# Performance work log

Hardware: AMD Instinct MI355X
Metric: run time of the kernel (lower is better)

Reference implementation:

```python
import jax, jax.numpy as jnp
import numpy as np
import math

B, S, H, D = 4, 4096, 2048, 128  # batch, seq_len, hidden_dim, head_size

def setup_inputs() -> dict:
    key = jax.random.key(0)
    ks = jax.random.split(key, 7)
    scale = 1.0 / math.sqrt(H)
    return {
        "x": jax.random.normal(ks[0], (B, S, H), dtype=jnp.float32),
        "Wq": jax.random.normal(ks[1], (H, D), dtype=jnp.float32) * scale,
        "bq": jnp.zeros((D,), dtype=jnp.float32),
        "Wk": jax.random.normal(ks[2], (H, D), dtype=jnp.float32) * scale,
        "bk": jnp.zeros((D,), dtype=jnp.float32),
        "Wv": jax.random.normal(ks[3], (H, D), dtype=jnp.float32) * scale,
        "bv": jnp.zeros((D,), dtype=jnp.float32),
    }

def reference(x, Wq, bq, Wk, bk, Wv, bv):
    # projections: [B,S,D]
    q = x @ Wq + bq
    k = x @ Wk + bk
    v = x @ Wv + bv
    # raw scores [B,S,S] with causal mask, NO pre-softmax scaling (as in source)
    scores = jnp.einsum('bsd,btd->bst', q, k)
    causal = jnp.tril(jnp.ones((S, S), dtype=bool))
    scores = jnp.where(causal, scores, -jnp.inf)
    # non-standard: scale AFTER softmax by 1/sqrt(head_size)
    w = jax.nn.softmax(scores, axis=-1) * (1.0 / math.sqrt(D))
    # dropout p=0.0 -> identity
    return jnp.einsum('bst,btd->bsd', w, v)
```

## Files before the change

### kernel.cpp

```cpp
#include <hip/hip_runtime.h>
#include <math.h>
#include <stdint.h>

#define SEQ   4096
#define HID   2048
#define HD    128
#define NROWS 16384

typedef __attribute__((ext_vector_type(8))) short bf16x8;
typedef __attribute__((ext_vector_type(4))) float f32x4;

static constexpr float OSCALE = 0.088388347648318447f;

using gvptr = const __attribute__((address_space(1))) void*;
using lvptr = __attribute__((address_space(3))) void*;
__device__ __forceinline__ void gld_lds16(const void* g, void* l) {
    __builtin_amdgcn_global_load_lds((gvptr)g, (lvptr)l, 16, 0, 0);
}

__device__ __forceinline__ unsigned short f2bf_rne(float f) {
    union { float f; unsigned u; } v; v.f = f;
    unsigned u = v.u + 0x7fffu + ((v.u >> 16) & 1u);
    return (unsigned short)(u >> 16);
}
__device__ __forceinline__ unsigned short f2bf_tr(float f) {
    union { float f; unsigned u; } v; v.f = f;
    return (unsigned short)(v.u >> 16);
}
__device__ __forceinline__ float bf2f(unsigned short h) {
    union { unsigned u; float f; } v; v.u = ((unsigned)h) << 16;
    return v.f;
}

__global__ __launch_bounds__(256) void prep_w(
    const float* __restrict__ Wq, const float* __restrict__ Wk, const float* __restrict__ Wv,
    unsigned short* __restrict__ wth, unsigned short* __restrict__ wtl)
{
    __shared__ float T[64][68];
    const int tid = threadIdx.x;
    const int k0 = blockIdx.x * 64, n0 = blockIdx.y * 64, mm = blockIdx.z;
    const float* W = (mm == 0) ? Wq : (mm == 1) ? Wk : Wv;
    #pragma unroll
    for (int i = 0; i < 4; ++i) {
        const int fi = i * 256 + tid, kk = fi >> 4, nc = (fi & 15) * 4;
        const float4 w = *(const float4*)(W + (size_t)(k0 + kk) * HD + n0 + nc);
        T[kk][nc] = w.x; T[kk][nc + 1] = w.y; T[kk][nc + 2] = w.z; T[kk][nc + 3] = w.w;
    }
    __syncthreads();
    unsigned short* oh = wth + (size_t)mm * HD * HID;
    unsigned short* ol = wtl + (size_t)mm * HD * HID;
    #pragma unroll
    for (int i = 0; i < 4; ++i) {
        const int fi = i * 256 + tid, nn = fi >> 4, kc = (fi & 15) * 4;
        const float a = T[kc][nn], b = T[kc + 1][nn], c = T[kc + 2][nn], d = T[kc + 3][nn];
        ushort4 hv, lv;
        hv.x = f2bf_rne(a); hv.y = f2bf_rne(b); hv.z = f2bf_rne(c); hv.w = f2bf_rne(d);
        lv.x = f2bf_rne(a - bf2f(hv.x)); lv.y = f2bf_rne(b - bf2f(hv.y));
        lv.z = f2bf_rne(c - bf2f(hv.z)); lv.w = f2bf_rne(d - bf2f(hv.w));
        *(ushort4*)(oh + (size_t)(n0 + nn) * HID + k0 + kc) = hv;
        *(ushort4*)(ol + (size_t)(n0 + nn) * HID + k0 + kc) = lv;
    }
}

__global__ __launch_bounds__(256, 3) void qkv_split(
    const float* __restrict__ x,
    const float* __restrict__ bq, const float* __restrict__ bk, const float* __restrict__ bv,
    const unsigned short* __restrict__ wth, const unsigned short* __restrict__ wtl,
    unsigned short* __restrict__ qh, unsigned short* __restrict__ ql,
    unsigned short* __restrict__ kh, unsigned short* __restrict__ kl,
    unsigned short* __restrict__ vth)
{
    __shared__ unsigned short Ah[64][64], Al[64][64];
    __shared__ unsigned short Bh[128][64], Bl[128][64];

    const int tid = threadIdx.x, wave = tid >> 6, lane = tid & 63;
    const int l15 = lane & 15, q4 = lane >> 4;
    const int wr = wave >> 1, wc = wave & 1;
    const int type = blockIdx.x % 3;
    const int tile = blockIdx.x / 3;
    const int r0 = tile * 64;
    const bool qk = (type < 2);

    const unsigned short* wh = wth + (size_t)type * HD * HID;
    const unsigned short* wl = wtl + (size_t)type * HD * HID;

    const int srow   = lane >> 3;
    const int schunk = ((lane & 7) ^ srow) * 8;

    f32x4 acc[2][4];
    #pragma unroll
    for (int mt = 0; mt < 2; ++mt)
        #pragma unroll
        for (int nt = 0; nt < 4; ++nt)
            acc[mt][nt] = (f32x4){0.f, 0.f, 0.f, 0.f};

    const float* xbase = x + (size_t)r0 * HID;

    float4 xv[4];
    #pragma unroll
    for (int i = 0; i < 4; ++i) {
        const int fi = i * 256 + tid, row = fi >> 4, kc = (fi & 15) * 4;
        xv[i] = *(const float4*)(xbase + (size_t)row * HID + kc);
    }

    for (int k0 = 0; k0 < HID; k0 += 64) {
        __syncthreads();

        {
            #pragma unroll
            for (int c = 0; c < 4; ++c) {
                const int row = wave * 32 + c * 8;
                gld_lds16(wh + (size_t)(row + srow) * HID + k0 + schunk, &Bh[row][0]);
            }
            if (qk) {
                #pragma unroll
                for (int c = 0; c < 4; ++c) {
                    const int row = wave * 32 + c * 8;
                    gld_lds16(wl + (size_t)(row + srow) * HID + k0 + schunk, &Bl[row][0]);
                }
            }
        }
        #pragma unroll
        for (int i = 0; i < 4; ++i) {
            const int fi = i * 256 + tid, row = fi >> 4, kc = (fi & 15) * 4;
            const int pk = ((kc >> 3) ^ (row & 7)) * 8 + (kc & 7);
            ushort4 hv;
            hv.x = f2bf_tr(xv[i].x); hv.y = f2bf_tr(xv[i].y);
            hv.z = f2bf_tr(xv[i].z); hv.w = f2bf_tr(xv[i].w);
            *(ushort4*)&Ah[row][pk] = hv;
            if (qk) {
                ushort4 lv;
                lv.x = f2bf_tr(xv[i].x - bf2f(hv.x)); lv.y = f2bf_tr(xv[i].y - bf2f(hv.y));
                lv.z = f2bf_tr(xv[i].z - bf2f(hv.z)); lv.w = f2bf_tr(xv[i].w - bf2f(hv.w));
                *(ushort4*)&Al[row][pk] = lv;
            }
        }
        __syncthreads();

        const int kn = (k0 + 64 < HID) ? (k0 + 64) : 0;
        #pragma unroll
        for (int i = 0; i < 4; ++i) {
            const int fi = i * 256 + tid, row = fi >> 4, kc = (fi & 15) * 4;
            xv[i] = *(const float4*)(xbase + (size_t)row * HID + kn + kc);
        }

        #pragma unroll
        for (int ks = 0; ks < 2; ++ks) {
            const int pc = ((ks * 4 + q4) ^ (l15 & 7)) * 8;
            bf16x8 ah[2], al[2];
            #pragma unroll
            for (int mt = 0; mt < 2; ++mt) {
                const int ar = wr * 32 + mt * 16 + l15;
                ah[mt] = *(const bf16x8*)&Ah[ar][pc];
                if (qk) al[mt] = *(const bf16x8*)&Al[ar][pc];
            }
            #pragma unroll
            for (int nt = 0; nt < 4; ++nt) {
                const int br = wc * 64 + nt * 16 + l15;
                const bf16x8 bh = *(const bf16x8*)&Bh[br][pc];
                #pragma unroll
                for (int mt = 0; mt < 2; ++mt)
                    acc[mt][nt] = __builtin_amdgcn_mfma_f32_16x16x32_bf16(ah[mt], bh, acc[mt][nt], 0, 0, 0);
                if (qk) {
                    const bf16x8 bl = *(const bf16x8*)&Bl[br][pc];
                    #pragma unroll
                    for (int mt = 0; mt < 2; ++mt) {
                        acc[mt][nt] = __builtin_amdgcn_mfma_f32_16x16x32_bf16(ah[mt], bl, acc[mt][nt], 0, 0, 0);
                        acc[mt][nt] = __builtin_amdgcn_mfma_f32_16x16x32_bf16(al[mt], bh, acc[mt][nt], 0, 0, 0);
                    }
                }
            }
        }
    }

    if (qk) {
        const float* bb = (type == 0) ? bq : bk;
        unsigned short* oh = (type == 0) ? qh : kh;
        unsigned short* ol = (type == 0) ? ql : kl;
        #pragma unroll
        for (int nt = 0; nt < 4; ++nt) {
            const int col = wc * 64 + nt * 16 + l15;
            const float bias = bb[col];
            #pragma unroll
            for (int mt = 0; mt < 2; ++mt) {
                const int Rb = r0 + wr * 32 + mt * 16 + q4 * 4;
                #pragma unroll
                for (int r = 0; r < 4; ++r) {
                    const float v = acc[mt][nt][r] + bias;
                    const unsigned short h = f2bf_rne(v);
                    oh[(size_t)(Rb + r) * HD + col] = h;
                    ol[(size_t)(Rb + r) * HD + col] = f2bf_rne(v - bf2f(h));
                }
            }
        }
    } else {
        #pragma unroll
        for (int nt = 0; nt < 4; ++nt) {
            const int col = wc * 64 + nt * 16 + l15;
            const float bias = bv[col];
            #pragma unroll
            for (int mt = 0; mt < 2; ++mt) {
                const int Rb = r0 + wr * 32 + mt * 16 + q4 * 4;
                const int bi = Rb >> 12, s0 = Rb & 4095;
                ushort4 pv;
                pv.x = f2bf_rne(acc[mt][nt][0] + bias);
                pv.y = f2bf_rne(acc[mt][nt][1] + bias);
                pv.z = f2bf_rne(acc[mt][nt][2] + bias);
                pv.w = f2bf_rne(acc[mt][nt][3] + bias);
                *(ushort4*)(vth + ((size_t)(bi * HD + col)) * SEQ + s0) = pv;
            }
        }
    }
}

__global__ __launch_bounds__(256, 2) void flash_mfma(
    const unsigned short* __restrict__ qh, const unsigned short* __restrict__ ql,
    const unsigned short* __restrict__ kh, const unsigned short* __restrict__ kl,
    const unsigned short* __restrict__ vth,
    unsigned short* __restrict__ oPb, float* __restrict__ mP, float* __restrict__ lP)
{
    __shared__ unsigned short Kh[64][128], Kl[64][128];
    __shared__ unsigned short Vt[128][64];
    __shared__ unsigned short Ps[4][16][72];

    const int tid = threadIdx.x, wave = tid >> 6, lane = tid & 63;
    const int l15 = lane & 15, q4 = lane >> 4;
    const int h = blockIdx.x & 3, pair = (blockIdx.x >> 2) & 31, b = blockIdx.x >> 7;

    const int krow_l = lane >> 4;
    const int vrow_l = lane >> 3;
    const int vsc = ((lane & 7) ^ (vrow_l & 7)) * 8;
    const int kkey7 = l15 & 7;
    const int vkey7 = l15 & 7;

    for (int side = 0; side < 2; ++side) {
        const int tt = side ? (63 - pair) : pair;
        const int n = tt + 1;
        const int j0 = (n * h) >> 2, j1 = (n * (h + 1)) >> 2;

        const int qrow = b * SEQ + tt * 64 + wave * 16 + l15;
        bf16x8 aqh[4], aql[4];
        #pragma unroll
        for (int ks = 0; ks < 4; ++ks) {
            aqh[ks] = *(const bf16x8*)(qh + (size_t)qrow * HD + ks * 32 + q4 * 8);
            aql[ks] = *(const bf16x8*)(ql + (size_t)qrow * HD + ks * 32 + q4 * 8);
        }
        f32x4 oa[8];
        #pragma unroll
        for (int d = 0; d < 8; ++d) oa[d] = (f32x4){0.f, 0.f, 0.f, 0.f};
        float m_r[4] = {-INFINITY, -INFINITY, -INFINITY, -INFINITY};
        float l_r[4] = {0.f, 0.f, 0.f, 0.f};

        for (int j = j0; j < j1; ++j) {
            __syncthreads();
            {
                const size_t kb = (size_t)b * SEQ + j * 64;
                #pragma unroll
                for (int c = 0; c < 4; ++c) {
                    const int rl = c * 4 + krow_l;
                    const int sc = (l15 ^ (rl & 7)) * 8;
                    const size_t gr = (kb + wave * 16 + rl) * HD + sc;
                    gld_lds16(kh + gr, &Kh[wave * 16 + c * 4][0]);
                    gld_lds16(kl + gr, &Kl[wave * 16 + c * 4][0]);
                }
                #pragma unroll
                for (int c = 0; c < 4; ++c)
                    gld_lds16(vth + ((size_t)(b * HD + wave * 32 + c * 8 + vrow_l)) * SEQ
                                  + j * 64 + vsc,
                              &Vt[wave * 32 + c * 8][0]);
            }
            __syncthreads();

            f32x4 s[4];
            #pragma unroll
            for (int nt = 0; nt < 4; ++nt) s[nt] = (f32x4){0.f, 0.f, 0.f, 0.f};
            #pragma unroll
            for (int ks = 0; ks < 4; ++ks) {
                const int pc = ((ks * 4 + q4) ^ kkey7) * 8;
                #pragma unroll
                for (int nt = 0; nt < 4; ++nt) {
                    const bf16x8 bh = *(const bf16x8*)&Kh[nt * 16 + l15][pc];
                    const bf16x8 bl = *(const bf16x8*)&Kl[nt * 16 + l15][pc];
                    s[nt] = __builtin_amdgcn_mfma_f32_16x16x32_bf16(aqh[ks], bh, s[nt], 0, 0, 0);
                    s[nt] = __builtin_amdgcn_mfma_f32_16x16x32_bf16(aql[ks], bh, s[nt], 0, 0, 0);
                    s[nt] = __builtin_amdgcn_mfma_f32_16x16x32_bf16(aqh[ks], bl, s[nt], 0, 0, 0);
                }
            }
            if (j == tt) {
                #pragma unroll
                for (int nt = 0; nt < 4; ++nt) {
                    const int cl = nt * 16 + l15;
                    #pragma unroll
                    for (int r = 0; r < 4; ++r) {
                        const int rl = wave * 16 + q4 * 4 + r;
                        if (cl > rl) s[nt][r] = -INFINITY;
                    }
                }
            }
            #pragma unroll
            for (int r = 0; r < 4; ++r) {
                float mt = fmaxf(fmaxf(s[0][r], s[1][r]), fmaxf(s[2][r], s[3][r]));
                mt = fmaxf(mt, __shfl_xor(mt, 1));
                mt = fmaxf(mt, __shfl_xor(mt, 2));
                mt = fmaxf(mt, __shfl_xor(mt, 4));
                mt = fmaxf(mt, __shfl_xor(mt, 8));
                const float mn = fmaxf(m_r[r], mt);
                const float al = __expf(m_r[r] - mn);
                m_r[r] = mn;
                const float p0 = __expf(s[0][r] - mn), p1 = __expf(s[1][r] - mn);
                const float p2 = __expf(s[2][r] - mn), p3 = __expf(s[3][r] - mn);
                Ps[wave][q4 * 4 + r][l15]      = f2bf_tr(p0);
                Ps[wave][q4 * 4 + r][16 + l15] = f2bf_tr(p1);
                Ps[wave][q4 * 4 + r][32 + l15] = f2bf_tr(p2);
                Ps[wave][q4 * 4 + r][48 + l15] = f2bf_tr(p3);
                float ps = p0 + p1 + p2 + p3;
                ps += __shfl_xor(ps, 1); ps += __shfl_xor(ps, 2);
                ps += __shfl_xor(ps, 4); ps += __shfl_xor(ps, 8);
                l_r[r] = l_r[r] * al + ps;
                #pragma unroll
                for (int d = 0; d < 8; ++d) oa[d][r] *= al;
            }
            const bf16x8 ap0 = *(const bf16x8*)&Ps[wave][l15][q4 * 8];
            const bf16x8 ap1 = *(const bf16x8*)&Ps[wave][l15][32 + q4 * 8];
            #pragma unroll
            for (int d = 0; d < 8; ++d) {
                const bf16x8 bv0 = *(const bf16x8*)&Vt[d * 16 + l15][(q4 ^ vkey7) * 8];
                const bf16x8 bv1 = *(const bf16x8*)&Vt[d * 16 + l15][((4 + q4) ^ vkey7) * 8];
                oa[d] = __builtin_amdgcn_mfma_f32_16x16x32_bf16(ap0, bv0, oa[d], 0, 0, 0);
                oa[d] = __builtin_amdgcn_mfma_f32_16x16x32_bf16(ap1, bv1, oa[d], 0, 0, 0);
            }
        }

        const int R0 = b * SEQ + tt * 64 + wave * 16 + q4 * 4;
        unsigned short* op = oPb + (size_t)h * NROWS * HD;
        #pragma unroll
        for (int d = 0; d < 8; ++d)
            #pragma unroll
            for (int r = 0; r < 4; ++r)
                op[(size_t)(R0 + r) * HD + d * 16 + l15] = f2bf_rne(oa[d][r]);
        if (l15 == 0) {
            #pragma unroll
            for (int r = 0; r < 4; ++r) {
                mP[h * NROWS + R0 + r] = m_r[r];
                lP[h * NROWS + R0 + r] = l_r[r];
            }
        }
    }
}

__global__ __launch_bounds__(256) void flash_merge(
    const unsigned short* __restrict__ oPb, const float* __restrict__ mP,
    const float* __restrict__ lP, float* __restrict__ out)
{
    const int idx = blockIdx.x * 256 + threadIdx.x;
    const int r = idx >> 5, c = (idx & 31) * 4;
    float m[4], l[4];
    #pragma unroll
    for (int i = 0; i < 4; ++i) { m[i] = mP[i * NROWS + r]; l[i] = lP[i * NROWS + r]; }
    float M = fmaxf(fmaxf(m[0], m[1]), fmaxf(m[2], m[3]));
    float a[4], lsum = 0.f;
    #pragma unroll
    for (int i = 0; i < 4; ++i) { a[i] = __expf(m[i] - M); lsum += l[i] * a[i]; }
    const float inv = OSCALE / lsum;
    float ox = 0.f, oy = 0.f, oz = 0.f, ow = 0.f;
    #pragma unroll
    for (int i = 0; i < 4; ++i) {
        const ushort4 ov = *(const ushort4*)(oPb + (size_t)i * NROWS * HD + (size_t)r * HD + c);
        ox += a[i] * bf2f(ov.x); oy += a[i] * bf2f(ov.y);
        oz += a[i] * bf2f(ov.z); ow += a[i] * bf2f(ov.w);
    }
    float4 o; o.x = ox * inv; o.y = oy * inv; o.z = oz * inv; o.w = ow * inv;
    *(float4*)(out + (size_t)r * HD + c) = o;
}

extern "C" void kernel_launch(void* const* d_in, const int* in_sizes, int n_in,
                              void* d_out, int out_size, void* d_ws, size_t ws_size,
                              hipStream_t stream)
{
    (void)in_sizes; (void)n_in; (void)out_size; (void)ws_size;
    const float* x  = (const float*)d_in[0];
    const float* Wq = (const float*)d_in[1];
    const float* bq = (const float*)d_in[2];
    const float* Wk = (const float*)d_in[3];
    const float* bk = (const float*)d_in[4];
    const float* Wv = (const float*)d_in[5];
    const float* bv = (const float*)d_in[6];
    float* out = (float*)d_out;

    char* w = (char*)d_ws;
    unsigned short* qh  = (unsigned short*)(w);
    unsigned short* ql  = (unsigned short*)(w + 4194304);
    unsigned short* kh  = (unsigned short*)(w + 8388608);
    unsigned short* kl  = (unsigned short*)(w + 12582912);
    unsigned short* vth = (unsigned short*)(w + 16777216);
    unsigned short* wth = (unsigned short*)(w + 20971520);
    unsigned short* wtl = (unsigned short*)(w + 22544384);
    unsigned short* oPb = (unsigned short*)(w + 24117248);
    float* mP = (float*)(w + 40894464);
    float* lP = (float*)(w + 41156608);

    prep_w<<<dim3(32, 2, 3), 256, 0, stream>>>(Wq, Wk, Wv, wth, wtl);
    qkv_split<<<768, 256, 0, stream>>>(x, bq, bk, bv, wth, wtl, qh, ql, kh, kl, vth);
    flash_mfma<<<512, 256, 0, stream>>>(qh, ql, kh, kl, vth, oPb, mP, lP);
    flash_merge<<<2048, 256, 0, stream>>>(oPb, mP, lP, out);
}
```

Measured before the change: 311.4 us.

## Double-buffer weight tiles in QKV projection and split Q/K blocks by column half

Rewrites the QKV projection kernel so weight tiles are double-buffered in a single shared buffer: the next K-slice is loaded asynchronously into LDS while the current one is consumed, with manual waitcnt and barriers. Q and K work, which needs three MFMAs per product for split-precision, is split into two 64-column halves, giving 1280 blocks instead of 768 to balance them against the cheaper V blocks. This adds more redundant reads of x across blocks and relies on hand-tuned vmcnt counts being correct.

```diff
diff --git a/kernel.cpp b/kernel.cpp
--- a/kernel.cpp
+++ b/kernel.cpp
@@ -62,7 +62,7 @@
     }
 }
 
-__global__ __launch_bounds__(256, 3) void qkv_split(
+__global__ __launch_bounds__(256, 3) void qkv_pipe(
     const float* __restrict__ x,
     const float* __restrict__ bq, const float* __restrict__ bk, const float* __restrict__ bv,
     const unsigned short* __restrict__ wth, const unsigned short* __restrict__ wtl,
@@ -70,19 +70,25 @@
     unsigned short* __restrict__ kh, unsigned short* __restrict__ kl,
     unsigned short* __restrict__ vth)
 {
-    __shared__ unsigned short Ah[64][64], Al[64][64];
-    __shared__ unsigned short Bh[128][64], Bl[128][64];
+    __shared__ unsigned short LB[24576];
 
     const int tid = threadIdx.x, wave = tid >> 6, lane = tid & 63;
     const int l15 = lane & 15, q4 = lane >> 4;
     const int wr = wave >> 1, wc = wave & 1;
-    const int type = blockIdx.x % 3;
-    const int tile = blockIdx.x / 3;
+    const int kind = blockIdx.x >> 8;
+    const int tile = blockIdx.x & 255;
     const int r0 = tile * 64;
-    const bool qk = (type < 2);
-
-    const unsigned short* wh = wth + (size_t)type * HD * HID;
-    const unsigned short* wl = wtl + (size_t)type * HD * HID;
+    const bool qk = (kind < 4);
+    const int type = qk ? (kind >> 1) : 2;
+    const int colbase = qk ? (kind & 1) * 64 : 0;
+
+    unsigned short* Ah = LB;
+    unsigned short* Al = LB + 4096;
+    unsigned short* B0 = LB + (qk ? 8192 : 4096);
+    const int bstride = qk ? 4096 : 8192;
+
+    const unsigned short* wh = wth + (size_t)type * HD * HID + (size_t)colbase * HID;
+    const unsigned short* wl = wtl + (size_t)type * HD * HID + (size_t)colbase * HID;
 
     const int srow   = lane >> 3;
     const int schunk = ((lane & 7) ^ srow) * 8;
@@ -98,78 +104,120 @@
 
     float4 xv[4];
     #pragma unroll
-    for (int i = 0; i < 4; ++i) {
-        const int fi = i * 256 + tid, row = fi >> 4, kc = (fi & 15) * 4;
-        xv[i] = *(const float4*)(xbase + (size_t)row * HID + kc);
-    }
-
-    for (int k0 = 0; k0 < HID; k0 += 64) {
-        __syncthreads();
-
-        {
+    for (int i4 = 0; i4 < 4; ++i4) {
+        const int fi = i4 * 256 + tid, row = fi >> 4, kc = (fi & 15) * 4;
+        xv[i4] = *(const float4*)(xbase + (size_t)row * HID + kc);
+    }
+
+    {
+        if (qk) {
+            unsigned short* bh = B0;
+            #pragma unroll
+            for (int c = 0; c < 2; ++c) {
+                const int row = wave * 16 + c * 8;
+                gld_lds16(wh + (size_t)(row + srow) * HID + schunk, bh + row * 64);
+                gld_lds16(wl + (size_t)(row + srow) * HID + schunk, bh + 8192 + row * 64);
+            }
+        } else {
+            unsigned short* bh = B0;
             #pragma unroll
             for (int c = 0; c < 4; ++c) {
                 const int row = wave * 32 + c * 8;
-                gld_lds16(wh + (size_t)(row + srow) * HID + k0 + schunk, &Bh[row][0]);
-            }
+                gld_lds16(wh + (size_t)(row + srow) * HID + schunk, bh + row * 64);
+            }
+        }
+    }
+
+    for (int i = 0; i < 32; ++i) {
+        const int k0 = i * 64, rb = i & 1;
+        const int kn = (k0 + 64 < HID) ? (k0 + 64) : 0;
+
+        __builtin_amdgcn_s_barrier();
+        __builtin_amdgcn_sched_barrier(0);
+
+        {
+            unsigned short* bdst = B0 + (rb ^ 1) * bstride;
             if (qk) {
+                #pragma unroll
+                for (int c = 0; c < 2; ++c) {
+                    const int row = wave * 16 + c * 8;
+                    gld_lds16(wh + (size_t)(row + srow) * HID + kn + schunk, bdst + row * 64);
+                    gld_lds16(wl + (size_t)(row + srow) * HID + kn + schunk, bdst + 8192 + row * 64);
+                }
+            } else {
                 #pragma unroll
                 for (int c = 0; c < 4; ++c) {
                     const int row = wave * 32 + c * 8;
-                    gld_lds16(wl + (size_t)(row + srow) * HID + k0 + schunk, &Bl[row][0]);
-                }
-            }
-        }
-        #pragma unroll
-        for (int i = 0; i < 4; ++i) {
-            const int fi = i * 256 + tid, row = fi >> 4, kc = (fi & 15) * 4;
+                    gld_lds16(wh + (size_t)(row + srow) * HID + kn + schunk, bdst + row * 64);
+                }
+            }
+        }
+
+        #pragma unroll
+        for (int i4 = 0; i4 < 4; ++i4) {
+            const int fi = i4 * 256 + tid, row = fi >> 4, kc = (fi & 15) * 4;
             const int pk = ((kc >> 3) ^ (row & 7)) * 8 + (kc & 7);
             ushort4 hv;
-            hv.x = f2bf_tr(xv[i].x); hv.y = f2bf_tr(xv[i].y);
-            hv.z = f2bf_tr(xv[i].z); hv.w = f2bf_tr(xv[i].w);
-            *(ushort4*)&Ah[row][pk] = hv;
+            hv.x = f2bf_tr(xv[i4].x); hv.y = f2bf_tr(xv[i4].y);
+            hv.z = f2bf_tr(xv[i4].z); hv.w = f2bf_tr(xv[i4].w);
+            *(ushort4*)(Ah + row * 64 + pk) = hv;
             if (qk) {
                 ushort4 lv;
-                lv.x = f2bf_tr(xv[i].x - bf2f(hv.x)); lv.y = f2bf_tr(xv[i].y - bf2f(hv.y));
-                lv.z = f2bf_tr(xv[i].z - bf2f(hv.z)); lv.w = f2bf_tr(xv[i].w - bf2f(hv.w));
-                *(ushort4*)&Al[row][pk] = lv;
-            }
-        }
-        __syncthreads();
-
-        const int kn = (k0 + 64 < HID) ? (k0 + 64) : 0;
-        #pragma unroll
-        for (int i = 0; i < 4; ++i) {
-            const int fi = i * 256 + tid, row = fi >> 4, kc = (fi & 15) * 4;
-            xv[i] = *(const float4*)(xbase + (size_t)row * HID + kn + kc);
-        }
-
-        #pragma unroll
-        for (int ks = 0; ks < 2; ++ks) {
-            const int pc = ((ks * 4 + q4) ^ (l15 & 7)) * 8;
-            bf16x8 ah[2], al[2];
-            #pragma unroll
-            for (int mt = 0; mt < 2; ++mt) {
-                const int ar = wr * 32 + mt * 16 + l15;
-                ah[mt] = *(const bf16x8*)&Ah[ar][pc];
-                if (qk) al[mt] = *(const bf16x8*)&Al[ar][pc];
-            }
-            #pragma unroll
-            for (int nt = 0; nt < 4; ++nt) {
-                const int br = wc * 64 + nt * 16 + l15;
-                const bf16x8 bh = *(const bf16x8*)&Bh[br][pc];
-                #pragma unroll
-                for (int mt = 0; mt < 2; ++mt)
-                    acc[mt][nt] = __builtin_amdgcn_mfma_f32_16x16x32_bf16(ah[mt], bh, acc[mt][nt], 0, 0, 0);
+                lv.x = f2bf_tr(xv[i4].x - bf2f(hv.x)); lv.y = f2bf_tr(xv[i4].y - bf2f(hv.y));
+                lv.z = f2bf_tr(xv[i4].z - bf2f(hv.z)); lv.w = f2bf_tr(xv[i4].w - bf2f(hv.w));
+                *(ushort4*)(Al + row * 64 + pk) = lv;
+            }
+        }
+
+        asm volatile("s_waitcnt vmcnt(4)" ::: "memory");
+        asm volatile("s_waitcnt lgkmcnt(0)" ::: "memory");
+        __builtin_amdgcn_s_barrier();
+        __builtin_amdgcn_sched_barrier(0);
+
+        {
+            const unsigned short* bhc = B0 + rb * bstride;
+            #pragma unroll
+            for (int ks = 0; ks < 2; ++ks) {
+                const int pc = ((ks * 4 + q4) ^ (l15 & 7)) * 8;
+                bf16x8 ah[2], al[2];
+                #pragma unroll
+                for (int mt = 0; mt < 2; ++mt) {
+                    const int ar = wr * 32 + mt * 16 + l15;
+                    ah[mt] = *(const bf16x8*)(Ah + ar * 64 + pc);
+                    if (qk) al[mt] = *(const bf16x8*)(Al + ar * 64 + pc);
+                }
                 if (qk) {
-                    const bf16x8 bl = *(const bf16x8*)&Bl[br][pc];
                     #pragma unroll
-                    for (int mt = 0; mt < 2; ++mt) {
-                        acc[mt][nt] = __builtin_amdgcn_mfma_f32_16x16x32_bf16(ah[mt], bl, acc[mt][nt], 0, 0, 0);
-                        acc[mt][nt] = __builtin_amdgcn_mfma_f32_16x16x32_bf16(al[mt], bh, acc[mt][nt], 0, 0, 0);
+                    for (int nt = 0; nt < 2; ++nt) {
+                        const int br = wc * 32 + nt * 16 + l15;
+                        const bf16x8 bh = *(const bf16x8*)(bhc + br * 64 + pc);
+                        const bf16x8 bl = *(const bf16x8*)(bhc + 8192 + br * 64 + pc);
+                        #pragma unroll
+                        for (int mt = 0; mt < 2; ++mt)
+                            acc[mt][nt] = __builtin_amdgcn_mfma_f32_16x16x32_bf16(ah[mt], bh, acc[mt][nt], 0, 0, 0);
+                        #pragma unroll
+                        for (int mt = 0; mt < 2; ++mt) {
+                            acc[mt][nt] = __builtin_amdgcn_mfma_f32_16x16x32_bf16(ah[mt], bl, acc[mt][nt], 0, 0, 0);
+                            acc[mt][nt] = __builtin_amdgcn_mfma_f32_16x16x32_bf16(al[mt], bh, acc[mt][nt], 0, 0, 0);
+                        }
                     }
-                }
-            }
+                } else {
+                    #pragma unroll
+                    for (int nt = 0; nt < 4; ++nt) {
+                        const int br = wc * 64 + nt * 16 + l15;
+                        const bf16x8 bh = *(const bf16x8*)(bhc + br * 64 + pc);
+                        #pragma unroll
+                        for (int mt = 0; mt < 2; ++mt)
+                            acc[mt][nt] = __builtin_amdgcn_mfma_f32_16x16x32_bf16(ah[mt], bh, acc[mt][nt], 0, 0, 0);
+                    }
+                }
+            }
+        }
+
+        #pragma unroll
+        for (int i4 = 0; i4 < 4; ++i4) {
+            const int fi = i4 * 256 + tid, row = fi >> 4, kc = (fi & 15) * 4;
+            xv[i4] = *(const float4*)(xbase + (size_t)row * HID + kn + kc);
         }
     }
 
@@ -178,8 +226,8 @@
         unsigned short* oh = (type == 0) ? qh : kh;
         unsigned short* ol = (type == 0) ? ql : kl;
         #pragma unroll
-        for (int nt = 0; nt < 4; ++nt) {
-            const int col = wc * 64 + nt * 16 + l15;
+        for (int nt = 0; nt < 2; ++nt) {
+            const int col = colbase + wc * 32 + nt * 16 + l15;
             const float bias = bb[col];
             #pragma unroll
             for (int mt = 0; mt < 2; ++mt) {
@@ -400,7 +448,7 @@
     float* lP = (float*)(w + 41156608);
 
     prep_w<<<dim3(32, 2, 3), 256, 0, stream>>>(Wq, Wk, Wv, wth, wtl);
-    qkv_split<<<768, 256, 0, stream>>>(x, bq, bk, bv, wth, wtl, qh, ql, kh, kl, vth);
+    qkv_pipe<<<1280, 256, 0, stream>>>(x, bq, bk, bv, wth, wtl, qh, ql, kh, kl, vth);
     flash_mfma<<<512, 256, 0, stream>>>(qh, ql, kh, kl, vth, oPb, mP, lP);
     flash_merge<<<2048, 256, 0, stream>>>(oPb, mP, lP, out);
 }
```

Result: slower. 339.2 us (+8.9%).

## Prefetch next K tile into registers and double-buffer V in LDS

Applied to the files above, without the earlier changes.

Restructures the flash attention inner loop to software-pipeline loads. The next K hi/lo tile is fetched into registers and written to LDS at the start of the next iteration, and V is double-buffered in LDS through async global-to-LDS loads. MFMA sections are wrapped in s_setprio to favour matrix issue. This hides global load latency behind compute, at the cost of more registers and LDS, which could lower occupancy under the 2-blocks launch bound.

```diff
diff --git a/kernel.cpp b/kernel.cpp
--- a/kernel.cpp
+++ b/kernel.cpp
@@ -220,7 +220,7 @@
     unsigned short* __restrict__ oPb, float* __restrict__ mP, float* __restrict__ lP)
 {
     __shared__ unsigned short Kh[64][128], Kl[64][128];
-    __shared__ unsigned short Vt[128][64];
+    __shared__ unsigned short Vt2[2][128][64];
     __shared__ unsigned short Ps[4][16][72];
 
     const int tid = threadIdx.x, wave = tid >> 6, lane = tid & 63;
@@ -251,29 +251,59 @@
         float m_r[4] = {-INFINITY, -INFINITY, -INFINITY, -INFINITY};
         float l_r[4] = {0.f, 0.f, 0.f, 0.f};
 
+        bf16x8 krh[4], krl[4];
+        if (j0 < j1) {
+            __syncthreads();
+            #pragma unroll
+            for (int c = 0; c < 4; ++c)
+                gld_lds16(vth + ((size_t)(b * HD + wave * 32 + c * 8 + vrow_l)) * SEQ
+                              + j0 * 64 + vsc,
+                          &Vt2[0][wave * 32 + c * 8][0]);
+            const size_t kb0 = (size_t)b * SEQ + j0 * 64;
+            #pragma unroll
+            for (int c = 0; c < 4; ++c) {
+                const int rl = c * 4 + krow_l;
+                const int sc = (l15 ^ (rl & 7)) * 8;
+                const size_t gr = (kb0 + wave * 16 + rl) * HD + sc;
+                krh[c] = *(const bf16x8*)(kh + gr);
+                krl[c] = *(const bf16x8*)(kl + gr);
+            }
+        }
+
+        int p = 0;
         for (int j = j0; j < j1; ++j) {
             __syncthreads();
+
+            #pragma unroll
+            for (int c = 0; c < 4; ++c) {
+                *(bf16x8*)(&Kh[wave * 16 + c * 4][0] + lane * 8) = krh[c];
+                *(bf16x8*)(&Kl[wave * 16 + c * 4][0] + lane * 8) = krl[c];
+            }
+
+            const int jn = (j + 1 < j1) ? (j + 1) : j;
+            #pragma unroll
+            for (int c = 0; c < 4; ++c)
+                gld_lds16(vth + ((size_t)(b * HD + wave * 32 + c * 8 + vrow_l)) * SEQ
+                              + jn * 64 + vsc,
+                          &Vt2[p ^ 1][wave * 32 + c * 8][0]);
             {
-                const size_t kb = (size_t)b * SEQ + j * 64;
+                const size_t kbn = (size_t)b * SEQ + jn * 64;
                 #pragma unroll
                 for (int c = 0; c < 4; ++c) {
                     const int rl = c * 4 + krow_l;
                     const int sc = (l15 ^ (rl & 7)) * 8;
-                    const size_t gr = (kb + wave * 16 + rl) * HD + sc;
-                    gld_lds16(kh + gr, &Kh[wave * 16 + c * 4][0]);
-                    gld_lds16(kl + gr, &Kl[wave * 16 + c * 4][0]);
-                }
-                #pragma unroll
-                for (int c = 0; c < 4; ++c)
-                    gld_lds16(vth + ((size_t)(b * HD + wave * 32 + c * 8 + vrow_l)) * SEQ
-                                  + j * 64 + vsc,
-                              &Vt[wave * 32 + c * 8][0]);
-            }
+                    const size_t gr = (kbn + wave * 16 + rl) * HD + sc;
+                    krh[c] = *(const bf16x8*)(kh + gr);
+                    krl[c] = *(const bf16x8*)(kl + gr);
+                }
+            }
+
             __syncthreads();
 
             f32x4 s[4];
             #pragma unroll
             for (int nt = 0; nt < 4; ++nt) s[nt] = (f32x4){0.f, 0.f, 0.f, 0.f};
+            __builtin_amdgcn_s_setprio(1);
             #pragma unroll
             for (int ks = 0; ks < 4; ++ks) {
                 const int pc = ((ks * 4 + q4) ^ kkey7) * 8;
@@ -286,6 +316,7 @@
                     s[nt] = __builtin_amdgcn_mfma_f32_16x16x32_bf16(aqh[ks], bl, s[nt], 0, 0, 0);
                 }
             }
+            __builtin_amdgcn_s_setprio(0);
             if (j == tt) {
                 #pragma unroll
                 for (int nt = 0; nt < 4; ++nt) {
@@ -322,13 +353,16 @@
             }
             const bf16x8 ap0 = *(const bf16x8*)&Ps[wave][l15][q4 * 8];
             const bf16x8 ap1 = *(const bf16x8*)&Ps[wave][l15][32 + q4 * 8];
+            __builtin_amdgcn_s_setprio(1);
             #pragma unroll
             for (int d = 0; d < 8; ++d) {
-                const bf16x8 bv0 = *(const bf16x8*)&Vt[d * 16 + l15][(q4 ^ vkey7) * 8];
-                const bf16x8 bv1 = *(const bf16x8*)&Vt[d * 16 + l15][((4 + q4) ^ vkey7) * 8];
+                const bf16x8 bv0 = *(const bf16x8*)&Vt2[p][d * 16 + l15][(q4 ^ vkey7) * 8];
+                const bf16x8 bv1 = *(const bf16x8*)&Vt2[p][d * 16 + l15][((4 + q4) ^ vkey7) * 8];
                 oa[d] = __builtin_amdgcn_mfma_f32_16x16x32_bf16(ap0, bv0, oa[d], 0, 0, 0);
                 oa[d] = __builtin_amdgcn_mfma_f32_16x16x32_bf16(ap1, bv1, oa[d], 0, 0, 0);
             }
+            __builtin_amdgcn_s_setprio(0);
+            p ^= 1;
         }
 
         const int R0 = b * SEQ + tt * 64 + wave * 16 + q4 * 4;
```

Measured after the change: 316.7 us. Within noise of the previous version (+1.7%).

## Split the QKV projection's K dimension across wave pairs and reduce through LDS

Applied to the files above, without the earlier changes.

The QKV projection kernel previously tiled the 64x128 output as a 2x2 grid of waves, each handling 32x64 over the full K range. Now each wave owns a 64x64 output half and a single 32-wide K slice of every 64-wide K chunk. Partial sums from the second K slice are reduced through reused LDS at the end. This lets each wave load all four A fragments once per K slice and reuse them across more MFMAs. The cost is doubling the accumulator registers to 64 floats per lane, which may hurt occupancy under launch_bounds(256,3), plus an extra LDS reduction and having only half the waves run the epilogue.

```diff
diff --git a/kernel.cpp b/kernel.cpp
--- a/kernel.cpp
+++ b/kernel.cpp
@@ -62,7 +62,7 @@
     }
 }
 
-__global__ __launch_bounds__(256, 3) void qkv_split(
+__global__ __launch_bounds__(256, 3) void qkv_ksplit(
     const float* __restrict__ x,
     const float* __restrict__ bq, const float* __restrict__ bk, const float* __restrict__ bv,
     const unsigned short* __restrict__ wth, const unsigned short* __restrict__ wtl,
@@ -70,12 +70,15 @@
     unsigned short* __restrict__ kh, unsigned short* __restrict__ kl,
     unsigned short* __restrict__ vth)
 {
-    __shared__ unsigned short Ah[64][64], Al[64][64];
-    __shared__ unsigned short Bh[128][64], Bl[128][64];
+    __shared__ unsigned short LDSB[24576];
+    unsigned short* Ah = LDSB;
+    unsigned short* Al = LDSB + 4096;
+    unsigned short* Bh = LDSB + 8192;
+    unsigned short* Bl = LDSB + 16384;
 
     const int tid = threadIdx.x, wave = tid >> 6, lane = tid & 63;
     const int l15 = lane & 15, q4 = lane >> 4;
-    const int wr = wave >> 1, wc = wave & 1;
+    const int kslice = wave >> 1, half = wave & 1;
     const int type = blockIdx.x % 3;
     const int tile = blockIdx.x / 3;
     const int r0 = tile * 64;
@@ -87,9 +90,9 @@
     const int srow   = lane >> 3;
     const int schunk = ((lane & 7) ^ srow) * 8;
 
-    f32x4 acc[2][4];
-    #pragma unroll
-    for (int mt = 0; mt < 2; ++mt)
+    f32x4 acc[4][4];
+    #pragma unroll
+    for (int mt = 0; mt < 4; ++mt)
         #pragma unroll
         for (int nt = 0; nt < 4; ++nt)
             acc[mt][nt] = (f32x4){0.f, 0.f, 0.f, 0.f};
@@ -103,6 +106,8 @@
         xv[i] = *(const float4*)(xbase + (size_t)row * HID + kc);
     }
 
+    const int pc = ((kslice * 4 + q4) ^ (l15 & 7)) * 8;
+
     for (int k0 = 0; k0 < HID; k0 += 64) {
         __syncthreads();
 
@@ -110,13 +115,13 @@
             #pragma unroll
             for (int c = 0; c < 4; ++c) {
                 const int row = wave * 32 + c * 8;
-                gld_lds16(wh + (size_t)(row + srow) * HID + k0 + schunk, &Bh[row][0]);
+                gld_lds16(wh + (size_t)(row + srow) * HID + k0 + schunk, Bh + row * 64);
             }
             if (qk) {
                 #pragma unroll
                 for (int c = 0; c < 4; ++c) {
                     const int row = wave * 32 + c * 8;
-                    gld_lds16(wl + (size_t)(row + srow) * HID + k0 + schunk, &Bl[row][0]);
+                    gld_lds16(wl + (size_t)(row + srow) * HID + k0 + schunk, Bl + row * 64);
                 }
             }
         }
@@ -127,12 +132,12 @@
             ushort4 hv;
             hv.x = f2bf_tr(xv[i].x); hv.y = f2bf_tr(xv[i].y);
             hv.z = f2bf_tr(xv[i].z); hv.w = f2bf_tr(xv[i].w);
-            *(ushort4*)&Ah[row][pk] = hv;
+            *(ushort4*)(Ah + row * 64 + pk) = hv;
             if (qk) {
                 ushort4 lv;
                 lv.x = f2bf_tr(xv[i].x - bf2f(hv.x)); lv.y = f2bf_tr(xv[i].y - bf2f(hv.y));
                 lv.z = f2bf_tr(xv[i].z - bf2f(hv.z)); lv.w = f2bf_tr(xv[i].w - bf2f(hv.w));
-                *(ushort4*)&Al[row][pk] = lv;
+                *(ushort4*)(Al + row * 64 + pk) = lv;
             }
         }
         __syncthreads();
@@ -144,70 +149,86 @@
             xv[i] = *(const float4*)(xbase + (size_t)row * HID + kn + kc);
         }
 
-        #pragma unroll
-        for (int ks = 0; ks < 2; ++ks) {
-            const int pc = ((ks * 4 + q4) ^ (l15 & 7)) * 8;
-            bf16x8 ah[2], al[2];
-            #pragma unroll
-            for (int mt = 0; mt < 2; ++mt) {
-                const int ar = wr * 32 + mt * 16 + l15;
-                ah[mt] = *(const bf16x8*)&Ah[ar][pc];
-                if (qk) al[mt] = *(const bf16x8*)&Al[ar][pc];
-            }
+        bf16x8 ah[4], al[4];
+        #pragma unroll
+        for (int mt = 0; mt < 4; ++mt) {
+            const int ar = mt * 16 + l15;
+            ah[mt] = *(const bf16x8*)(Ah + ar * 64 + pc);
+            if (qk) al[mt] = *(const bf16x8*)(Al + ar * 64 + pc);
+        }
+        #pragma unroll
+        for (int nt = 0; nt < 4; ++nt) {
+            const int br = half * 64 + nt * 16 + l15;
+            const bf16x8 bh = *(const bf16x8*)(Bh + br * 64 + pc);
+            #pragma unroll
+            for (int mt = 0; mt < 4; ++mt)
+                acc[mt][nt] = __builtin_amdgcn_mfma_f32_16x16x32_bf16(ah[mt], bh, acc[mt][nt], 0, 0, 0);
+            if (qk) {
+                const bf16x8 bl = *(const bf16x8*)(Bl + br * 64 + pc);
+                #pragma unroll
+                for (int mt = 0; mt < 4; ++mt) {
+                    acc[mt][nt] = __builtin_amdgcn_mfma_f32_16x16x32_bf16(ah[mt], bl, acc[mt][nt], 0, 0, 0);
+                    acc[mt][nt] = __builtin_amdgcn_mfma_f32_16x16x32_bf16(al[mt], bh, acc[mt][nt], 0, 0, 0);
+                }
+            }
+        }
+    }
+
+    __syncthreads();
+    float* red = (float*)LDSB;
+    if (kslice == 1) {
+        #pragma unroll
+        for (int mt = 0; mt < 4; ++mt)
+            #pragma unroll
+            for (int nt = 0; nt < 4; ++nt)
+                *(f32x4*)(red + (((half * 16 + mt * 4 + nt) * 64) + lane) * 4) = acc[mt][nt];
+    }
+    __syncthreads();
+    if (kslice == 0) {
+        #pragma unroll
+        for (int mt = 0; mt < 4; ++mt)
             #pragma unroll
             for (int nt = 0; nt < 4; ++nt) {
-                const int br = wc * 64 + nt * 16 + l15;
-                const bf16x8 bh = *(const bf16x8*)&Bh[br][pc];
-                #pragma unroll
-                for (int mt = 0; mt < 2; ++mt)
-                    acc[mt][nt] = __builtin_amdgcn_mfma_f32_16x16x32_bf16(ah[mt], bh, acc[mt][nt], 0, 0, 0);
-                if (qk) {
-                    const bf16x8 bl = *(const bf16x8*)&Bl[br][pc];
+                const f32x4 o = *(const f32x4*)(red + (((half * 16 + mt * 4 + nt) * 64) + lane) * 4);
+                acc[mt][nt] += o;
+            }
+
+        if (qk) {
+            const float* bb = (type == 0) ? bq : bk;
+            unsigned short* oh = (type == 0) ? qh : kh;
+            unsigned short* ol = (type == 0) ? ql : kl;
+            #pragma unroll
+            for (int nt = 0; nt < 4; ++nt) {
+                const int col = half * 64 + nt * 16 + l15;
+                const float bias = bb[col];
+                #pragma unroll
+                for (int mt = 0; mt < 4; ++mt) {
+                    const int Rb = r0 + mt * 16 + q4 * 4;
                     #pragma unroll
-                    for (int mt = 0; mt < 2; ++mt) {
-                        acc[mt][nt] = __builtin_amdgcn_mfma_f32_16x16x32_bf16(ah[mt], bl, acc[mt][nt], 0, 0, 0);
-                        acc[mt][nt] = __builtin_amdgcn_mfma_f32_16x16x32_bf16(al[mt], bh, acc[mt][nt], 0, 0, 0);
+                    for (int r = 0; r < 4; ++r) {
+                        const float v = acc[mt][nt][r] + bias;
+                        const unsigned short h = f2bf_rne(v);
+                        oh[(size_t)(Rb + r) * HD + col] = h;
+                        ol[(size_t)(Rb + r) * HD + col] = f2bf_rne(v - bf2f(h));
                     }
                 }
             }
-        }
-    }
-
-    if (qk) {
-        const float* bb = (type == 0) ? bq : bk;
-        unsigned short* oh = (type == 0) ? qh : kh;
-        unsigned short* ol = (type == 0) ? ql : kl;
-        #pragma unroll
-        for (int nt = 0; nt < 4; ++nt) {
-            const int col = wc * 64 + nt * 16 + l15;
-            const float bias = bb[col];
-            #pragma unroll
-            for (int mt = 0; mt < 2; ++mt) {
-                const int Rb = r0 + wr * 32 + mt * 16 + q4 * 4;
-                #pragma unroll
-                for (int r = 0; r < 4; ++r) {
-                    const float v = acc[mt][nt][r] + bias;
-                    const unsigned short h = f2bf_rne(v);
-                    oh[(size_t)(Rb + r) * HD + col] = h;
-                    ol[(size_t)(Rb + r) * HD + col] = f2bf_rne(v - bf2f(h));
-                }
-            }
-        }
-    } else {
-        #pragma unroll
-        for (int nt = 0; nt < 4; ++nt) {
-            const int col = wc * 64 + nt * 16 + l15;
-            const float bias = bv[col];
-            #pragma unroll
-            for (int mt = 0; mt < 2; ++mt) {
-                const int Rb = r0 + wr * 32 + mt * 16 + q4 * 4;
-                const int bi = Rb >> 12, s0 = Rb & 4095;
-                ushort4 pv;
-                pv.x = f2bf_rne(acc[mt][nt][0] + bias);
-                pv.y = f2bf_rne(acc[mt][nt][1] + bias);
-                pv.z = f2bf_rne(acc[mt][nt][2] + bias);
-                pv.w = f2bf_rne(acc[mt][nt][3] + bias);
-                *(ushort4*)(vth + ((size_t)(bi * HD + col)) * SEQ + s0) = pv;
+        } else {
+            #pragma unroll
+            for (int nt = 0; nt < 4; ++nt) {
+                const int col = half * 64 + nt * 16 + l15;
+                const float bias = bv[col];
+                #pragma unroll
+                for (int mt = 0; mt < 4; ++mt) {
+                    const int Rb = r0 + mt * 16 + q4 * 4;
+                    const int bi = Rb >> 12, s0 = Rb & 4095;
+                    ushort4 pv;
+                    pv.x = f2bf_rne(acc[mt][nt][0] + bias);
+                    pv.y = f2bf_rne(acc[mt][nt][1] + bias);
+                    pv.z = f2bf_rne(acc[mt][nt][2] + bias);
+                    pv.w = f2bf_rne(acc[mt][nt][3] + bias);
+                    *(ushort4*)(vth + ((size_t)(bi * HD + col)) * SEQ + s0) = pv;
+                }
             }
         }
     }
@@ -400,7 +421,7 @@
     float* lP = (float*)(w + 41156608);
 
     prep_w<<<dim3(32, 2, 3), 256, 0, stream>>>(Wq, Wk, Wv, wth, wtl);
-    qkv_split<<<768, 256, 0, stream>>>(x, bq, bk, bv, wth, wtl, qh, ql, kh, kl, vth);
+    qkv_ksplit<<<768, 256, 0, stream>>>(x, bq, bk, bv, wth, wtl, qh, ql, kh, kl, vth);
     flash_mfma<<<512, 256, 0, stream>>>(qh, ql, kh, kl, vth, oPb, mP, lP);
     flash_merge<<<2048, 256, 0, stream>>>(oPb, mP, lP, out);
 }
```

Result: no change. 310.8 us (-0.2%).
